# Performance work log

Measured on AMD Instinct MI355X. Metric: run time of the kernel, lower is better.

The kernel has to match this reference:

```python
import jax, jax.numpy as jnp
import numpy as np

N_NODES = 100000
D = 512
N_EDGES = 150000
N_PRED = 200000
EPS = 1e-12  # F.normalize default eps


def setup_inputs() -> dict:
    key = jax.random.key(0)
    ks = jax.random.split(key, 8)
    scale = 1.0 / np.sqrt(D)
    return {
        "x": jax.random.normal(ks[0], (N_NODES, D), dtype=jnp.float32),
        "edge_index": jax.random.randint(ks[1], (2, N_EDGES), 0, N_NODES, dtype=jnp.int64),
        "edge_weight": jax.random.uniform(ks[2], (N_EDGES,), dtype=jnp.float32),
        "pred_edges": jax.random.randint(ks[3], (2, N_PRED), 0, N_NODES, dtype=jnp.int64),
        "W1": jax.random.normal(ks[4], (D, D), dtype=jnp.float32) * scale,
        "b1": jnp.zeros((D,), jnp.float32),
        "W2": jax.random.normal(ks[5], (D, D), dtype=jnp.float32) * scale,
        "b2": jnp.zeros((D,), jnp.float32),
        "Wf": jax.random.normal(ks[6], (D, 2), dtype=jnp.float32) * scale,
        "bf": jnp.zeros((2,), jnp.float32),
    }


def gcn_conv(x, W, b, row, col, w, n):
    """PyG GCNConv with normalize=True: add self-loops (weight 1),
    symmetric deg^-1/2 normalization, message = norm * (xW)[row], scatter-add to col."""
    loop = jnp.arange(n)
    row2 = jnp.concatenate([row, loop])
    col2 = jnp.concatenate([col, loop])
    w2 = jnp.concatenate([w, jnp.ones((n,), x.dtype)])
    deg = jax.ops.segment_sum(w2, col2, num_segments=n)
    dinv = jnp.where(deg > 0, jax.lax.rsqrt(jnp.maximum(deg, EPS)), 0.0)
    norm = dinv[row2] * w2 * dinv[col2]  # [E+n]
    h = x @ W  # [n, out]
    out = jax.ops.segment_sum(norm[:, None] * h[row2], col2, num_segments=n)
    return out + b


def res_block(x, W, b, row, col, w, n):
    h = jax.nn.relu(gcn_conv(x, W, b, row, col, w, n))
    # dropout is identity in eval mode; then row-wise L2 normalize (F.normalize)
    nrm = jnp.maximum(jnp.linalg.norm(h, axis=1, keepdims=True), EPS)
    h = h / nrm
    return (h + x) * 0.5  # residual average (use_identity=True)


def reference(x, edge_index, edge_weight, pred_edges, W1, b1, W2, b2, Wf, bf):
    n = x.shape[0]
    row, col = edge_index[0], edge_index[1]
    h = res_block(x, W1, b1, row, col, edge_weight, n)
    h = res_block(h, W2, b2, row, col, edge_weight, n)
    h = gcn_conv(h, Wf, bf, row, col, edge_weight, n)
    h = jax.nn.log_softmax(h, axis=1)  # [n, 2]
    # DotProductPredictor, vectorized: h[u]*h[v]*(-1) per predictor edge
    return -(h[pred_edges[0]] * h[pred_edges[1]])  # [N_PRED, 2]
```

## Files before the change

kernel.cpp:

```cpp
#include <hip/hip_runtime.h>
#include <hip/hip_bf16.h>
#include <math.h>

typedef __bf16 bf16x8 __attribute__((ext_vector_type(8)));
typedef float f32x4 __attribute__((ext_vector_type(4)));
struct __align__(16) US8 { unsigned short v[8]; };

typedef __attribute__((address_space(1))) const unsigned short GUS;
typedef __attribute__((address_space(3))) unsigned short LUS;
static __device__ __forceinline__ void gload16(const unsigned short* g, unsigned short* l) {
    __builtin_amdgcn_global_load_lds((GUS*)g, (LUS*)l, 16, 0, 0);
}

static __device__ __forceinline__ unsigned short f2bf(float f) {
    unsigned int u = __float_as_uint(f);
    unsigned int r = (u + 0x7fffu + ((u >> 16) & 1u)) >> 16;
    return (unsigned short)r;
}

__global__ void init_kernel(float* deg, int* cnt, int* cursor, int M) {
    int i = blockIdx.x * 256 + threadIdx.x;
    if (i < M) { deg[i] = 1.0f; cnt[i] = 0; cursor[i] = 0; }
}
__global__ void deg_cnt_kernel(const int* __restrict__ ei, const float* __restrict__ ew,
                               float* deg, int* cnt, int E) {
    int e = blockIdx.x * 256 + threadIdx.x;
    if (e < E) {
        int c = ei[E + e];
        atomicAdd(&deg[c], ew[e]);
        atomicAdd(&cnt[c], 1);
    }
}
__global__ void dinv_kernel(const float* __restrict__ deg, float* dinv, int M) {
    int i = blockIdx.x * 256 + threadIdx.x;
    if (i < M) dinv[i] = rsqrtf(deg[i]);
}

__global__ void chunk_sum_kernel(const int* __restrict__ cnt, int* partial, int M) {
    __shared__ int sd[256];
    int t = threadIdx.x;
    int i = blockIdx.x * 256 + t;
    sd[t] = (i < M) ? cnt[i] : 0;
    __syncthreads();
    for (int s = 128; s > 0; s >>= 1) {
        if (t < s) sd[t] += sd[t + s];
        __syncthreads();
    }
    if (t == 0) partial[blockIdx.x] = sd[0];
}
__global__ void scan_partial_kernel(int* partial, int NB) {
    __shared__ int sd[512];
    int t = threadIdx.x;
    int v = (t < NB) ? partial[t] : 0;
    sd[t] = v;
    __syncthreads();
    for (int o = 1; o < 512; o <<= 1) {
        int add = (t >= o) ? sd[t - o] : 0;
        __syncthreads();
        sd[t] += add;
        __syncthreads();
    }
    if (t < NB) partial[t] = sd[t] - v;
}
__global__ void rowptr_kernel(const int* __restrict__ cnt, const int* __restrict__ partial,
                              int* rowptr, int M, int E) {
    __shared__ int sd[256];
    int t = threadIdx.x;
    int i = blockIdx.x * 256 + t;
    int v = (i < M) ? cnt[i] : 0;
    sd[t] = v;
    __syncthreads();
    for (int o = 1; o < 256; o <<= 1) {
        int add = (t >= o) ? sd[t - o] : 0;
        __syncthreads();
        sd[t] += add;
        __syncthreads();
    }
    if (i < M) rowptr[i] = partial[blockIdx.x] + sd[t] - v;
    if (i == M - 1) rowptr[M] = E;
}
__global__ void csr_fill_kernel(const int* __restrict__ ei, const float* __restrict__ ew,
                                const float* __restrict__ dinv, const int* __restrict__ rowptr,
                                int* cursor, int* src, float* cf, int E) {
    int e = blockIdx.x * 256 + threadIdx.x;
    if (e < E) {
        int r = ei[e], c = ei[E + e];
        int k = atomicAdd(&cursor[c], 1);
        int pos = rowptr[c] + k;
        src[pos] = r;
        cf[pos] = dinv[r] * ew[e] * dinv[c];
    }
}

__global__ void agg_gather_kernel(const float* __restrict__ xin, const int* __restrict__ rowptr,
                                  const int* __restrict__ src, const float* __restrict__ cf,
                                  const float* __restrict__ dinv,
                                  unsigned short* __restrict__ abf, int M) {
    int row = blockIdx.x * 4 + (threadIdx.x >> 6);
    if (row >= M) return;
    int lane = threadIdx.x & 63;
    const float4* xp = (const float4*)(xin + (size_t)row * 512 + lane * 8);
    float d = dinv[row];
    float s = d * d;
    float4 v0 = xp[0], v1 = xp[1];
    float4 a0, a1;
    a0.x = s * v0.x; a0.y = s * v0.y; a0.z = s * v0.z; a0.w = s * v0.w;
    a1.x = s * v1.x; a1.y = s * v1.y; a1.z = s * v1.z; a1.w = s * v1.w;
    int beg = rowptr[row], end = rowptr[row + 1];
    for (int j = beg; j < end; j++) {
        int r = src[j];
        float coef = cf[j];
        const float4* rp = (const float4*)(xin + (size_t)r * 512 + lane * 8);
        float4 u0 = rp[0], u1 = rp[1];
        a0.x += coef * u0.x; a0.y += coef * u0.y; a0.z += coef * u0.z; a0.w += coef * u0.w;
        a1.x += coef * u1.x; a1.y += coef * u1.y; a1.z += coef * u1.z; a1.w += coef * u1.w;
    }
    US8 o;
    o.v[0] = f2bf(a0.x); o.v[1] = f2bf(a0.y); o.v[2] = f2bf(a0.z); o.v[3] = f2bf(a0.w);
    o.v[4] = f2bf(a1.x); o.v[5] = f2bf(a1.y); o.v[6] = f2bf(a1.z); o.v[7] = f2bf(a1.w);
    *(US8*)(abf + (size_t)row * 512 + lane * 8) = o;
}

__global__ void transpose_cvt_kernel(const float* __restrict__ W, unsigned short* __restrict__ BT) {
    int idx = blockIdx.x * 256 + threadIdx.x;
    int n = idx >> 9, k = idx & 511;
    BT[idx] = f2bf(W[k * 512 + n]);
}

__global__ __launch_bounds__(512, 4) void gemm_epi_kernel(
    const unsigned short* __restrict__ A,
    const unsigned short* __restrict__ BT,
    const float* __restrict__ bias,
    const float* __restrict__ xin,
    float* __restrict__ outp,
    int M) {
    __shared__ __align__(16) unsigned short As[64 * 32];
    __shared__ __align__(16) unsigned short Bs[512 * 32];
    __shared__ float red[8 * 64];
    __shared__ float invn[64];

    const int tid  = threadIdx.x;
    const int m0   = blockIdx.x * 64;
    const int wave = tid >> 6;
    const int lane = tid & 63;
    const int q    = lane >> 4;
    const int r    = lane & 15;

    f32x4 acc[4][4];
    #pragma unroll
    for (int mt = 0; mt < 4; mt++)
        #pragma unroll
        for (int nt = 0; nt < 4; nt++) acc[mt][nt] = (f32x4){0.f, 0.f, 0.f, 0.f};

    const int fr  = (r + (r >> 2)) & 3;
    const int kcp = q ^ fr;

    for (int ks = 0; ks < 16; ks++) {
        const int k0 = ks * 32;
        #pragma unroll
        for (int j = 0; j < 4; j++) {
            int c0 = j * 512 + wave * 64;
            int c  = c0 + lane;
            if (c0 < 256) {
                int row = c >> 2, kl = c & 3;
                int kc = kl ^ ((row + (row >> 2)) & 3);
                gload16(A + (((size_t)(m0 + row)) << 9) + k0 + kc * 8, As + c0 * 8);
            } else {
                int cb = c - 256, cb0 = c0 - 256;
                int n = cb >> 2, kl = cb & 3;
                int kc = kl ^ ((n + (n >> 2)) & 3);
                gload16(BT + (((size_t)n) << 9) + k0 + kc * 8, Bs + cb0 * 8);
            }
        }
        if (wave < 4) {
            int cb0 = 1792 + wave * 64;
            int cb = cb0 + lane;
            int n = cb >> 2, kl = cb & 3;
            int kc = kl ^ ((n + (n >> 2)) & 3);
            gload16(BT + (((size_t)n) << 9) + k0 + kc * 8, Bs + cb0 * 8);
        }
        __syncthreads();

        bf16x8 af[4];
        #pragma unroll
        for (int mt = 0; mt < 4; mt++)
            af[mt] = __builtin_bit_cast(bf16x8,
                *(const US8*)&As[((mt * 16 + r) << 5) + kcp * 8]);
        #pragma unroll
        for (int nt = 0; nt < 4; nt++) {
            bf16x8 bfr = __builtin_bit_cast(bf16x8,
                *(const US8*)&Bs[((wave * 64 + nt * 16 + r) << 5) + kcp * 8]);
            #pragma unroll
            for (int mt = 0; mt < 4; mt++)
                acc[mt][nt] = __builtin_amdgcn_mfma_f32_16x16x32_bf16(af[mt], bfr, acc[mt][nt], 0, 0, 0);
        }
        __syncthreads();
    }

    float bs[4];
    #pragma unroll
    for (int nt = 0; nt < 4; nt++) bs[nt] = bias[wave * 64 + nt * 16 + r];

    float ss[4][4];
    #pragma unroll
    for (int mt = 0; mt < 4; mt++) {
        #pragma unroll
        for (int reg = 0; reg < 4; reg++) {
            float s = 0.f;
            #pragma unroll
            for (int nt = 0; nt < 4; nt++) {
                float t = fmaxf(acc[mt][nt][reg] + bs[nt], 0.f);
                acc[mt][nt][reg] = t;
                s += t * t;
            }
            ss[mt][reg] = s;
        }
    }
    #pragma unroll
    for (int mt = 0; mt < 4; mt++)
        #pragma unroll
        for (int reg = 0; reg < 4; reg++) {
            float s = ss[mt][reg];
            s += __shfl_xor(s, 1, 64);
            s += __shfl_xor(s, 2, 64);
            s += __shfl_xor(s, 4, 64);
            s += __shfl_xor(s, 8, 64);
            ss[mt][reg] = s;
        }
    if (r == 0) {
        #pragma unroll
        for (int mt = 0; mt < 4; mt++)
            #pragma unroll
            for (int reg = 0; reg < 4; reg++)
                red[wave * 64 + mt * 16 + q * 4 + reg] = ss[mt][reg];
    }
    __syncthreads();
    if (tid < 64) {
        float s = 0.f;
        #pragma unroll
        for (int w = 0; w < 8; w++) s += red[w * 64 + tid];
        invn[tid] = 1.0f / fmaxf(sqrtf(s), 1e-12f);
    }
    __syncthreads();

    #pragma unroll
    for (int mt = 0; mt < 4; mt++) {
        #pragma unroll
        for (int reg = 0; reg < 4; reg++) {
            int m = mt * 16 + q * 4 + reg;
            int gm = m0 + m;
            if (gm < M) {
                float inv = invn[m];
                #pragma unroll
                for (int nt = 0; nt < 4; nt++) {
                    int col = wave * 64 + nt * 16 + r;
                    size_t idx = ((size_t)gm << 9) + col;
                    outp[idx] = (acc[mt][nt][reg] * inv + xin[idx]) * 0.5f;
                }
            }
        }
    }
}

__global__ void proj_kernel(const float* __restrict__ x3, const float* __restrict__ Wf,
                            float* __restrict__ p, int M) {
    __shared__ float w0[512], w1[512];
    int tid = threadIdx.x;
    for (int j = tid; j < 512; j += 256) { w0[j] = Wf[j * 2]; w1[j] = Wf[j * 2 + 1]; }
    __syncthreads();
    int row = blockIdx.x * 4 + (tid >> 6);
    if (row >= M) return;
    int lane = tid & 63;
    const float4* xp = (const float4*)(x3 + (size_t)row * 512 + lane * 8);
    float4 a = xp[0], b = xp[1];
    int j0 = lane * 8;
    float s0 = a.x * w0[j0] + a.y * w0[j0 + 1] + a.z * w0[j0 + 2] + a.w * w0[j0 + 3]
             + b.x * w0[j0 + 4] + b.y * w0[j0 + 5] + b.z * w0[j0 + 6] + b.w * w0[j0 + 7];
    float s1 = a.x * w1[j0] + a.y * w1[j0 + 1] + a.z * w1[j0 + 2] + a.w * w1[j0 + 3]
             + b.x * w1[j0 + 4] + b.y * w1[j0 + 5] + b.z * w1[j0 + 6] + b.w * w1[j0 + 7];
    #pragma unroll
    for (int off = 32; off > 0; off >>= 1) {
        s0 += __shfl_xor(s0, off, 64);
        s1 += __shfl_xor(s1, off, 64);
    }
    if (lane == 0) { p[row * 2] = s0; p[row * 2 + 1] = s1; }
}

__global__ void final_self_kernel(const float* __restrict__ p, const float* __restrict__ dinv,
                                  float* pa, int M) {
    int i = blockIdx.x * 256 + threadIdx.x;
    if (i < M) {
        float d = dinv[i]; float s = d * d;
        pa[i * 2] = s * p[i * 2];
        pa[i * 2 + 1] = s * p[i * 2 + 1];
    }
}
__global__ void final_edge_kernel(const float* __restrict__ p, const int* __restrict__ ei,
                                  const float* __restrict__ ew, const float* __restrict__ dinv,
                                  float* pa, int E) {
    int e = blockIdx.x * 256 + threadIdx.x;
    if (e < E) {
        int r = ei[e], c = ei[E + e];
        float coef = dinv[r] * ew[e] * dinv[c];
        atomicAdd(&pa[c * 2], coef * p[r * 2]);
        atomicAdd(&pa[c * 2 + 1], coef * p[r * 2 + 1]);
    }
}
__global__ void lsm_kernel(const float* __restrict__ pa, const float* __restrict__ bfv,
                           float* __restrict__ logp, int M) {
    int i = blockIdx.x * 256 + threadIdx.x;
    if (i < M) {
        float a = pa[i * 2] + bfv[0], b = pa[i * 2 + 1] + bfv[1];
        float m = fmaxf(a, b);
        float lse = m + logf(expf(a - m) + expf(b - m));
        logp[i * 2] = a - lse;
        logp[i * 2 + 1] = b - lse;
    }
}
__global__ void pred_kernel(const float* __restrict__ logp, const int* __restrict__ pe,
                            float* __restrict__ out, int P) {
    int i = blockIdx.x * 256 + threadIdx.x;
    if (i < P) {
        int u = pe[i], v = pe[P + i];
        out[i * 2]     = -(logp[u * 2] * logp[v * 2]);
        out[i * 2 + 1] = -(logp[u * 2 + 1] * logp[v * 2 + 1]);
    }
}

extern "C" void kernel_launch(void* const* d_in, const int* in_sizes, int n_in,
                              void* d_out, int out_size, void* d_ws, size_t ws_size,
                              hipStream_t stream) {
    const float* x   = (const float*)d_in[0];
    const int*   ei  = (const int*)d_in[1];
    const float* ew  = (const float*)d_in[2];
    const int*   pe  = (const int*)d_in[3];
    const float* W1  = (const float*)d_in[4];
    const float* b1  = (const float*)d_in[5];
    const float* W2  = (const float*)d_in[6];
    const float* b2  = (const float*)d_in[7];
    const float* Wf  = (const float*)d_in[8];
    const float* bfv = (const float*)d_in[9];
    float* out = (float*)d_out;

    const int M = in_sizes[0] / 512;
    const int E = in_sizes[2];
    const int P = in_sizes[3] / 2;
    const int NB = (M + 255) / 256;
    const int MB64 = (M + 63) / 64;
    const int Mpad = MB64 * 64;

    char* ws = (char*)d_ws;
    size_t off = 0;
    auto alloc = [&](size_t bytes) { void* q = ws + off; off += (bytes + 255) & ~(size_t)255; return q; };
    float* deg    = (float*)alloc((size_t)M * 4);
    float* dinv   = (float*)alloc((size_t)M * 4);
    int*   cnt    = (int*)alloc((size_t)M * 4);
    int*   cursor = (int*)alloc((size_t)M * 4);
    int*   rowptr = (int*)alloc((size_t)(M + 1) * 4);
    int*   partial= (int*)alloc((size_t)NB * 4);
    int*   srcidx = (int*)alloc((size_t)E * 4);
    float* cf     = (float*)alloc((size_t)E * 4);
    float* A      = (float*)alloc((size_t)M * 512 * 4);
    float* G      = (float*)alloc((size_t)M * 512 * 4);
    unsigned short* abf = (unsigned short*)alloc((size_t)Mpad * 512 * 2);
    unsigned short* BT1 = (unsigned short*)alloc(512 * 512 * 2);
    unsigned short* BT2 = (unsigned short*)alloc(512 * 512 * 2);
    float* p    = (float*)alloc((size_t)M * 2 * 4);
    float* pa   = (float*)alloc((size_t)M * 2 * 4);
    float* logp = (float*)alloc((size_t)M * 2 * 4);

    const int nthr = 256;

    init_kernel<<<NB, nthr, 0, stream>>>(deg, cnt, cursor, M);
    deg_cnt_kernel<<<(E + 255) / 256, nthr, 0, stream>>>(ei, ew, deg, cnt, E);
    dinv_kernel<<<NB, nthr, 0, stream>>>(deg, dinv, M);
    chunk_sum_kernel<<<NB, nthr, 0, stream>>>(cnt, partial, M);
    scan_partial_kernel<<<1, 512, 0, stream>>>(partial, NB);
    rowptr_kernel<<<NB, nthr, 0, stream>>>(cnt, partial, rowptr, M, E);
    csr_fill_kernel<<<(E + 255) / 256, nthr, 0, stream>>>(ei, ew, dinv, rowptr, cursor, srcidx, cf, E);
    transpose_cvt_kernel<<<1024, nthr, 0, stream>>>(W1, BT1);
    transpose_cvt_kernel<<<1024, nthr, 0, stream>>>(W2, BT2);

    agg_gather_kernel<<<(M + 3) / 4, nthr, 0, stream>>>(x, rowptr, srcidx, cf, dinv, abf, M);
    gemm_epi_kernel<<<MB64, 512, 0, stream>>>(abf, BT1, b1, x, G, M);

    agg_gather_kernel<<<(M + 3) / 4, nthr, 0, stream>>>(G, rowptr, srcidx, cf, dinv, abf, M);
    gemm_epi_kernel<<<MB64, 512, 0, stream>>>(abf, BT2, b2, G, A, M);

    proj_kernel<<<(M + 3) / 4, nthr, 0, stream>>>(A, Wf, p, M);
    final_self_kernel<<<NB, nthr, 0, stream>>>(p, dinv, pa, M);
    final_edge_kernel<<<(E + 255) / 256, nthr, 0, stream>>>(p, ei, ew, dinv, pa, E);
    lsm_kernel<<<NB, nthr, 0, stream>>>(pa, bfv, logp, M);
    pred_kernel<<<(P + 255) / 256, nthr, 0, stream>>>(logp, pe, out, P);
}
```

Baseline: 885.6 us.

## Store intermediate node features in bf16 to halve gather and epilogue traffic

Converts the input features to bf16 once and keeps the residual-block outputs in bf16. The gather, GEMM epilogue and projection kernels read and write bf16 instead of fp32. This is meant to cut the memory bandwidth spent on the large per-node feature arrays in the memory-bound gather and epilogue stages. It adds an extra conversion pass and loses precision in the residual path, and the epilogue now issues 2-byte scalar stores.

```diff
diff --git a/kernel.cpp b/kernel.cpp
--- a/kernel.cpp
+++ b/kernel.cpp
@@ -16,6 +16,22 @@
     unsigned int u = __float_as_uint(f);
     unsigned int r = (u + 0x7fffu + ((u >> 16) & 1u)) >> 16;
     return (unsigned short)r;
+}
+static __device__ __forceinline__ float bf2f(unsigned short u) {
+    return __uint_as_float(((unsigned int)u) << 16);
+}
+
+__global__ void cvt_bf16_kernel(const float* __restrict__ in, unsigned short* __restrict__ outb,
+                                int total8) {
+    int i = blockIdx.x * 256 + threadIdx.x;
+    if (i < total8) {
+        const float4* p = (const float4*)(in + (size_t)i * 8);
+        float4 a = p[0], b = p[1];
+        US8 o;
+        o.v[0] = f2bf(a.x); o.v[1] = f2bf(a.y); o.v[2] = f2bf(a.z); o.v[3] = f2bf(a.w);
+        o.v[4] = f2bf(b.x); o.v[5] = f2bf(b.y); o.v[6] = f2bf(b.z); o.v[7] = f2bf(b.w);
+        *(US8*)(outb + (size_t)i * 8) = o;
+    }
 }
 
 __global__ void init_kernel(float* deg, int* cnt, int* cursor, int M) {
@@ -92,33 +108,31 @@
     }
 }
 
-__global__ void agg_gather_kernel(const float* __restrict__ xin, const int* __restrict__ rowptr,
+__global__ void agg_gather_kernel(const unsigned short* __restrict__ xin, const int* __restrict__ rowptr,
                                   const int* __restrict__ src, const float* __restrict__ cf,
                                   const float* __restrict__ dinv,
                                   unsigned short* __restrict__ abf, int M) {
     int row = blockIdx.x * 4 + (threadIdx.x >> 6);
     if (row >= M) return;
     int lane = threadIdx.x & 63;
-    const float4* xp = (const float4*)(xin + (size_t)row * 512 + lane * 8);
+    US8 v = *(const US8*)(xin + ((size_t)row << 9) + lane * 8);
     float d = dinv[row];
     float s = d * d;
-    float4 v0 = xp[0], v1 = xp[1];
-    float4 a0, a1;
-    a0.x = s * v0.x; a0.y = s * v0.y; a0.z = s * v0.z; a0.w = s * v0.w;
-    a1.x = s * v1.x; a1.y = s * v1.y; a1.z = s * v1.z; a1.w = s * v1.w;
+    float a[8];
+    #pragma unroll
+    for (int t = 0; t < 8; t++) a[t] = s * bf2f(v.v[t]);
     int beg = rowptr[row], end = rowptr[row + 1];
     for (int j = beg; j < end; j++) {
         int r = src[j];
         float coef = cf[j];
-        const float4* rp = (const float4*)(xin + (size_t)r * 512 + lane * 8);
-        float4 u0 = rp[0], u1 = rp[1];
-        a0.x += coef * u0.x; a0.y += coef * u0.y; a0.z += coef * u0.z; a0.w += coef * u0.w;
-        a1.x += coef * u1.x; a1.y += coef * u1.y; a1.z += coef * u1.z; a1.w += coef * u1.w;
+        US8 u = *(const US8*)(xin + ((size_t)r << 9) + lane * 8);
+        #pragma unroll
+        for (int t = 0; t < 8; t++) a[t] += coef * bf2f(u.v[t]);
     }
     US8 o;
-    o.v[0] = f2bf(a0.x); o.v[1] = f2bf(a0.y); o.v[2] = f2bf(a0.z); o.v[3] = f2bf(a0.w);
-    o.v[4] = f2bf(a1.x); o.v[5] = f2bf(a1.y); o.v[6] = f2bf(a1.z); o.v[7] = f2bf(a1.w);
-    *(US8*)(abf + (size_t)row * 512 + lane * 8) = o;
+    #pragma unroll
+    for (int t = 0; t < 8; t++) o.v[t] = f2bf(a[t]);
+    *(US8*)(abf + ((size_t)row << 9) + lane * 8) = o;
 }
 
 __global__ void transpose_cvt_kernel(const float* __restrict__ W, unsigned short* __restrict__ BT) {
@@ -131,8 +145,8 @@
     const unsigned short* __restrict__ A,
     const unsigned short* __restrict__ BT,
     const float* __restrict__ bias,
-    const float* __restrict__ xin,
-    float* __restrict__ outp,
+    const unsigned short* __restrict__ xin,
+    unsigned short* __restrict__ outp,
     int M) {
     __shared__ __align__(16) unsigned short As[64 * 32];
     __shared__ __align__(16) unsigned short Bs[512 * 32];
@@ -255,14 +269,14 @@
                 for (int nt = 0; nt < 4; nt++) {
                     int col = wave * 64 + nt * 16 + r;
                     size_t idx = ((size_t)gm << 9) + col;
-                    outp[idx] = (acc[mt][nt][reg] * inv + xin[idx]) * 0.5f;
+                    outp[idx] = f2bf((acc[mt][nt][reg] * inv + bf2f(xin[idx])) * 0.5f);
                 }
             }
         }
     }
 }
 
-__global__ void proj_kernel(const float* __restrict__ x3, const float* __restrict__ Wf,
+__global__ void proj_kernel(const unsigned short* __restrict__ x3, const float* __restrict__ Wf,
                             float* __restrict__ p, int M) {
     __shared__ float w0[512], w1[512];
     int tid = threadIdx.x;
@@ -271,13 +285,15 @@
     int row = blockIdx.x * 4 + (tid >> 6);
     if (row >= M) return;
     int lane = tid & 63;
-    const float4* xp = (const float4*)(x3 + (size_t)row * 512 + lane * 8);
-    float4 a = xp[0], b = xp[1];
+    US8 v = *(const US8*)(x3 + ((size_t)row << 9) + lane * 8);
     int j0 = lane * 8;
-    float s0 = a.x * w0[j0] + a.y * w0[j0 + 1] + a.z * w0[j0 + 2] + a.w * w0[j0 + 3]
-             + b.x * w0[j0 + 4] + b.y * w0[j0 + 5] + b.z * w0[j0 + 6] + b.w * w0[j0 + 7];
-    float s1 = a.x * w1[j0] + a.y * w1[j0 + 1] + a.z * w1[j0 + 2] + a.w * w1[j0 + 3]
-             + b.x * w1[j0 + 4] + b.y * w1[j0 + 5] + b.z * w1[j0 + 6] + b.w * w1[j0 + 7];
+    float s0 = 0.f, s1 = 0.f;
+    #pragma unroll
+    for (int t = 0; t < 8; t++) {
+        float a = bf2f(v.v[t]);
+        s0 += a * w0[j0 + t];
+        s1 += a * w1[j0 + t];
+    }
     #pragma unroll
     for (int off = 32; off > 0; off >>= 1) {
         s0 += __shfl_xor(s0, off, 64);
@@ -360,8 +376,9 @@
     int*   partial= (int*)alloc((size_t)NB * 4);
     int*   srcidx = (int*)alloc((size_t)E * 4);
     float* cf     = (float*)alloc((size_t)E * 4);
-    float* A      = (float*)alloc((size_t)M * 512 * 4);
-    float* G      = (float*)alloc((size_t)M * 512 * 4);
+    unsigned short* xb  = (unsigned short*)alloc((size_t)M * 512 * 2);
+    unsigned short* x2b = (unsigned short*)alloc((size_t)M * 512 * 2);
+    unsigned short* x3b = (unsigned short*)alloc((size_t)M * 512 * 2);
     unsigned short* abf = (unsigned short*)alloc((size_t)Mpad * 512 * 2);
     unsigned short* BT1 = (unsigned short*)alloc(512 * 512 * 2);
     unsigned short* BT2 = (unsigned short*)alloc(512 * 512 * 2);
@@ -371,6 +388,7 @@
 
     const int nthr = 256;
 
+    cvt_bf16_kernel<<<(M * 64 + 255) / 256, nthr, 0, stream>>>(x, xb, M * 64);
     init_kernel<<<NB, nthr, 0, stream>>>(deg, cnt, cursor, M);
     deg_cnt_kernel<<<(E + 255) / 256, nthr, 0, stream>>>(ei, ew, deg, cnt, E);
     dinv_kernel<<<NB, nthr, 0, stream>>>(deg, dinv, M);
@@ -381,13 +399,13 @@
     transpose_cvt_kernel<<<1024, nthr, 0, stream>>>(W1, BT1);
     transpose_cvt_kernel<<<1024, nthr, 0, stream>>>(W2, BT2);
 
-    agg_gather_kernel<<<(M + 3) / 4, nthr, 0, stream>>>(x, rowptr, srcidx, cf, dinv, abf, M);
-    gemm_epi_kernel<<<MB64, 512, 0, stream>>>(abf, BT1, b1, x, G, M);
-
-    agg_gather_kernel<<<(M + 3) / 4, nthr, 0, stream>>>(G, rowptr, srcidx, cf, dinv, abf, M);
-    gemm_epi_kernel<<<MB64, 512, 0, stream>>>(abf, BT2, b2, G, A, M);
-
-    proj_kernel<<<(M + 3) / 4, nthr, 0, stream>>>(A, Wf, p, M);
+    agg_gather_kernel<<<(M + 3) / 4, nthr, 0, stream>>>(xb, rowptr, srcidx, cf, dinv, abf, M);
+    gemm_epi_kernel<<<MB64, 512, 0, stream>>>(abf, BT1, b1, xb, x2b, M);
+
+    agg_gather_kernel<<<(M + 3) / 4, nthr, 0, stream>>>(x2b, rowptr, srcidx, cf, dinv, abf, M);
+    gemm_epi_kernel<<<MB64, 512, 0, stream>>>(abf, BT2, b2, x2b, x3b, M);
+
+    proj_kernel<<<(M + 3) / 4, nthr, 0, stream>>>(x3b, Wf, p, M);
     final_self_kernel<<<NB, nthr, 0, stream>>>(p, dinv, pa, M);
     final_edge_kernel<<<(E + 255) / 256, nthr, 0, stream>>>(p, ei, ew, dinv, pa, E);
     lsm_kernel<<<NB, nthr, 0, stream>>>(pa, bfv, logp, M);
```

Measured after the change: 786.5 us. 1.13x faster.
